# Kernel optimization log

Hardware: AMD Instinct MI355X
Metric: run time of the kernel (lower is better)

## Reference

```python
import jax, jax.numpy as jnp
import numpy as np

B, H, S, D = 2, 12, 2048, 64

def setup_inputs() -> dict:
    key = jax.random.key(0)
    kq, kk, kv = jax.random.split(key, 3)
    Q = jax.random.normal(kq, (B, H, S, D), dtype=jnp.float32)
    K = jax.random.normal(kk, (B, H, S, D), dtype=jnp.float32)
    V = jax.random.normal(kv, (B, H, S, D), dtype=jnp.float32)
    return {"Q": Q, "K": K, "V": V}

def reference(Q, K, V):
    # NOTE: original code scales by sqrt(Q.shape[-2]) (the sequence length),
    # not the head dim — reproduced faithfully.
    scale = 1.0 / np.sqrt(Q.shape[-2]).astype(np.float32)
    scores = jnp.einsum('bhqd,bhkd->bhqk', Q, K) * scale  # [B,H,S,S]
    attn = jax.nn.softmax(scores, axis=-1)
    context = jnp.einsum('bhqk,bhkd->bhqd', attn, V)      # [B,H,S,D]
    # torch .squeeze(-1) only removes the last dim if it is size 1; D=64 so no-op
    return context
```

## Files before the change

### kernel.cpp

```cpp
#include <hip/hip_runtime.h>
#include <hip/hip_bf16.h>
#include <math.h>
#include <stdint.h>

#define BATCH 2
#define NH 12
#define SEQ 2048
#define HD 64
#define TQ 64
#define TK 64
#define NHEADS (BATCH*NH)
#define NIT (SEQ / TK)

typedef short bf16x8 __attribute__((ext_vector_type(8)));
typedef float f32x4 __attribute__((ext_vector_type(4)));
typedef float f32x16 __attribute__((ext_vector_type(16)));
typedef unsigned short us4_t __attribute__((ext_vector_type(4)));
typedef unsigned short us8_t __attribute__((ext_vector_type(8)));
typedef unsigned int u32x4 __attribute__((ext_vector_type(4)));

#if __has_builtin(__builtin_amdgcn_exp2f)
#define EXP2F(x) __builtin_amdgcn_exp2f(x)
#else
#define EXP2F(x) exp2f(x)
#endif

static __device__ __forceinline__ unsigned short f2bf(float f) {
    unsigned int u = __float_as_uint(f);
    u += 0x7fffu + ((u >> 16) & 1u);
    return (unsigned short)(u >> 16);
}

static __device__ __forceinline__ unsigned int pack2bf(float a, float b) {
    __hip_bfloat162 v = __float22bfloat162_rn(float2{a, b});
    return *(unsigned int*)&v;
}

static __device__ __forceinline__ void async_cp16(const void* g, void* l) {
    __builtin_amdgcn_global_load_lds(
        (const __attribute__((address_space(1))) void*)g,
        (__attribute__((address_space(3))) void*)(uintptr_t)l,
        16, 0, 0);
}

static __device__ __forceinline__ int tile_off(int r, int c) {
    int rp  = r >> 1;
    int pos = (((r & 1) << 3) | c) ^ (rp & 15);
    return rp * 128 + pos * 8;
}

__global__ __launch_bounds__(256)
void prep_kv(const float* __restrict__ K, const float* __restrict__ V,
             unsigned short* __restrict__ Kb, unsigned short* __restrict__ Vtb) {
    __shared__ unsigned short T[64][66];
    const int bh = blockIdx.x >> 5;
    const int s0 = (blockIdx.x & 31) * 64;
    const int tid = threadIdx.x;
    const size_t off = ((size_t)bh * SEQ + s0) * HD;

    #pragma unroll
    for (int u = 0; u < 4; ++u) {
        int idx = u * 1024 + tid * 4;
        float4 a = *(const float4*)&K[off + idx];
        us4_t r4 = { f2bf(a.x), f2bf(a.y), f2bf(a.z), f2bf(a.w) };
        *(us4_t*)&Kb[off + idx] = r4;
    }
    #pragma unroll
    for (int u = 0; u < 4; ++u) {
        int idx = u * 1024 + tid * 4;
        int r = idx >> 6, col = idx & 63;
        float4 a = *(const float4*)&V[off + idx];
        *(unsigned int*)&T[r][col]     = pack2bf(a.x, a.y);
        *(unsigned int*)&T[r][col + 2] = pack2bf(a.z, a.w);
    }
    __syncthreads();
    unsigned short* Vdst = Vtb + (size_t)bh * HD * SEQ;
    const int g = tid & 7, dd = tid >> 3;
    #pragma unroll
    for (int h = 0; h < 2; ++h) {
        int d = dd + 32 * h;
        us8_t r8;
        #pragma unroll
        for (int j = 0; j < 8; ++j) {
            int src = ((g >> 1) << 4) + ((j >> 2) << 3) + ((g & 1) << 2) + (j & 3);
            r8[j] = T[src][d];
        }
        *(us8_t*)&Vdst[(size_t)d * SEQ + s0 + g * 8] = r8;
    }
}

__global__ __launch_bounds__(256, 3)
void fa_main(const float* __restrict__ Q,
             const unsigned short* __restrict__ Kb,
             const unsigned short* __restrict__ Vtb,
             float* __restrict__ O, float qs) {
    const int x  = blockIdx.x & 7;
    const int t  = blockIdx.x >> 3;
    const int bh = x + 8 * (t % 3);
    const int qt = t / 3;
    const int q0 = qt * TQ;

    __shared__ __align__(16) unsigned char SH[49664];
    float* Lsum = (float*)(SH + 49152);
    float* Linv = (float*)(SH + 49408);
    float* ORed = (float*)SH;
    unsigned short* QS = (unsigned short*)(SH + 32768);

    const int tid  = threadIdx.x;
    const int w    = tid >> 6;
    const int mt   = w >> 1;
    const int nt   = w & 1;
    const int lane = tid & 63;
    const int l31  = lane & 31;
    const int hi   = lane >> 5;

    const float*          Qh = Q   + ((size_t)bh * SEQ + q0) * HD;
    const unsigned short* Kh = Kb  + (size_t)bh * SEQ * HD;
    const unsigned short* Vh = Vtb + (size_t)bh * HD * SEQ;

    int rS[2], cS[2];
    #pragma unroll
    for (int i = 0; i < 2; ++i) {
        int rp = w * 8 + 4 * i + (lane >> 4);
        int lc = (lane & 15) ^ (rp & 15);
        rS[i] = 2 * rp + (lc >> 3);
        cS[i] = lc & 7;
    }
    const int dst0 = (w * 8 + 0) * 128, dst1 = (w * 8 + 4) * 128;
    const size_t kG0 = (size_t)rS[0] * HD  + cS[0] * 8;
    const size_t kG1 = (size_t)rS[1] * HD  + cS[1] * 8;
    const size_t vG0 = (size_t)rS[0] * SEQ + cS[0] * 8;
    const size_t vG1 = (size_t)rS[1] * SEQ + cS[1] * 8;

    {
        unsigned short* K0 = (unsigned short*)(SH);
        unsigned short* V0 = (unsigned short*)(SH + 8192);
        async_cp16(Kh + kG0, &K0[dst0]);
        async_cp16(Kh + kG1, &K0[dst1]);
        async_cp16(Vh + vG0, &V0[dst0]);
        async_cp16(Vh + vG1, &V0[dst1]);
    }
    #pragma unroll
    for (int u = 0; u < 4; ++u) {
        int idx = u * 1024 + tid * 4;
        int r = idx >> 6, col = idx & 63;
        float4 a = *(const float4*)&Qh[idx];
        uint2 pk = { pack2bf(a.x * qs, a.y * qs), pack2bf(a.z * qs, a.w * qs) };
        *(uint2*)&QS[tile_off(r, col >> 3) + (col & 7)] = pk;
    }
    __syncthreads();

    bf16x8 qf[4];
    #pragma unroll
    for (int s = 0; s < 4; ++s)
        qf[s] = *(const bf16x8*)&QS[tile_off(mt * 32 + l31, s * 2 + hi)];
    __syncthreads();

    {
        unsigned short* K1 = (unsigned short*)(SH + 16384);
        unsigned short* V1 = (unsigned short*)(SH + 16384 + 8192);
        async_cp16(Kh + (size_t)TK * HD + kG0, &K1[dst0]);
        async_cp16(Kh + (size_t)TK * HD + kG1, &K1[dst1]);
        async_cp16(Vh + (size_t)TK + vG0,      &V1[dst0]);
        async_cp16(Vh + (size_t)TK + vG1,      &V1[dst1]);
    }

    int kOffL[4], vOffL[2][2];
    #pragma unroll
    for (int s = 0; s < 4; ++s) kOffL[s] = tile_off(nt * 32 + l31, s * 2 + hi);
    #pragma unroll
    for (int dt = 0; dt < 2; ++dt)
        #pragma unroll
        for (int ks = 0; ks < 2; ++ks)
            vOffL[dt][ks] = tile_off(dt * 32 + l31, nt * 4 + ks * 2 + hi);

    f32x16 o[2];
    o[0] = (f32x16)(0.f);
    o[1] = (f32x16)(0.f);
    float lsum = 0.f;

    auto FIN = [&](const f32x16& sp, const bf16x8 (&vp)[2][2]) {
        float e0[8], e1[8];
        #pragma unroll
        for (int r = 0; r < 8; ++r) e0[r] = EXP2F(sp[r]);
        #pragma unroll
        for (int r = 0; r < 8; ++r) e1[r] = EXP2F(sp[8 + r]);
        union { u32x4 d; bf16x8 h; } pu0, pu1;
        pu0.d = (u32x4){ pack2bf(e0[0], e0[1]), pack2bf(e0[2], e0[3]),
                         pack2bf(e0[4], e0[5]), pack2bf(e0[6], e0[7]) };
        pu1.d = (u32x4){ pack2bf(e1[0], e1[1]), pack2bf(e1[2], e1[3]),
                         pack2bf(e1[4], e1[5]), pack2bf(e1[6], e1[7]) };
        bf16x8 pf0 = pu0.h, pf1 = pu1.h;
        o[0] = __builtin_amdgcn_mfma_f32_32x32x16_bf16(pf0, vp[0][0], o[0], 0, 0, 0);
        o[1] = __builtin_amdgcn_mfma_f32_32x32x16_bf16(pf0, vp[1][0], o[1], 0, 0, 0);
        o[0] = __builtin_amdgcn_mfma_f32_32x32x16_bf16(pf1, vp[0][1], o[0], 0, 0, 0);
        o[1] = __builtin_amdgcn_mfma_f32_32x32x16_bf16(pf1, vp[1][1], o[1], 0, 0, 0);
        float t0 = ((e0[0] + e0[1]) + (e0[2] + e0[3]))
                 + ((e0[4] + e0[5]) + (e0[6] + e0[7]));
        float t1 = ((e1[0] + e1[1]) + (e1[2] + e1[3]))
                 + ((e1[4] + e1[5]) + (e1[6] + e1[7]));
        lsum += t0 + t1;
    };

    unsigned int b0 = 0, b1 = 16384, b2 = 32768;

    f32x16 scp;
    bf16x8 vfp[2][2];

    {
        unsigned short* Kn = (unsigned short*)(SH + b2);
        unsigned short* Vn = (unsigned short*)(SH + b2 + 8192);
        async_cp16(Kh + (size_t)2 * TK * HD + kG0, &Kn[dst0]);
        async_cp16(Kh + (size_t)2 * TK * HD + kG1, &Kn[dst1]);
        async_cp16(Vh + (size_t)2 * TK + vG0,      &Vn[dst0]);
        async_cp16(Vh + (size_t)2 * TK + vG1,      &Vn[dst1]);

        const unsigned short* Ks = (const unsigned short*)(SH + b0);
        const unsigned short* Vs = (const unsigned short*)(SH + b0 + 8192);
        #pragma unroll
        for (int dt = 0; dt < 2; ++dt)
            #pragma unroll
            for (int ks = 0; ks < 2; ++ks)
                vfp[dt][ks] = *(const bf16x8*)&Vs[vOffL[dt][ks]];
        f32x16 sc = (f32x16)(0.f);
        #pragma unroll
        for (int s = 0; s < 4; ++s) {
            bf16x8 kf = *(const bf16x8*)&Ks[kOffL[s]];
            sc = __builtin_amdgcn_mfma_f32_32x32x16_bf16(kf, qf[s], sc, 0, 0, 0);
        }
        scp = sc;
        unsigned int btmp = b0; b0 = b1; b1 = b2; b2 = btmp;
    }

    #pragma unroll 2
    for (int it = 1; it < NIT; ++it) {
        asm volatile("s_waitcnt lgkmcnt(0)" ::: "memory");
        if (it == NIT - 1) { asm volatile("s_waitcnt vmcnt(0)" ::: "memory"); }
        else               { asm volatile("s_waitcnt vmcnt(4)" ::: "memory"); }
        __builtin_amdgcn_s_barrier();

        if (it + 2 < NIT) {
            const size_t kv = (size_t)(it + 2) * TK;
            unsigned short* Kn = (unsigned short*)(SH + b2);
            unsigned short* Vn = (unsigned short*)(SH + b2 + 8192);
            async_cp16(Kh + kv * HD + kG0, &Kn[dst0]);
            async_cp16(Kh + kv * HD + kG1, &Kn[dst1]);
            async_cp16(Vh + kv + vG0,      &Vn[dst0]);
            async_cp16(Vh + kv + vG1,      &Vn[dst1]);
        }
        const unsigned short* Ks = (const unsigned short*)(SH + b0);
        const unsigned short* Vs = (const unsigned short*)(SH + b0 + 8192);

        bf16x8 vfc[2][2];
        #pragma unroll
        for (int dt = 0; dt < 2; ++dt)
            #pragma unroll
            for (int ks = 0; ks < 2; ++ks)
                vfc[dt][ks] = *(const bf16x8*)&Vs[vOffL[dt][ks]];

        f32x16 scc = (f32x16)(0.f);
        #pragma unroll
        for (int s = 0; s < 4; ++s) {
            bf16x8 kf = *(const bf16x8*)&Ks[kOffL[s]];
            scc = __builtin_amdgcn_mfma_f32_32x32x16_bf16(kf, qf[s], scc, 0, 0, 0);
        }
        FIN(scp, vfp);

        scp = scc;
        #pragma unroll
        for (int dt = 0; dt < 2; ++dt)
            #pragma unroll
            for (int ks = 0; ks < 2; ++ks)
                vfp[dt][ks] = vfc[dt][ks];

        unsigned int btmp = b0; b0 = b1; b1 = b2; b2 = btmp;
    }

    FIN(scp, vfp);

    lsum += __shfl_xor(lsum, 32, 64);

    if (nt == 1) {
        if (lane < 32) Lsum[mt * 32 + lane] = lsum;
        #pragma unroll
        for (int dt = 0; dt < 2; ++dt) {
            const int d = dt * 32 + l31;
            #pragma unroll
            for (int g = 0; g < 4; ++g) {
                const int m0 = mt * 32 + 8 * g + 4 * hi;
                const int ph = (m0 >> 2) ^ (d & 15);
                float4 v = { o[dt][4*g+0], o[dt][4*g+1], o[dt][4*g+2], o[dt][4*g+3] };
                *(float4*)&ORed[d * 64 + ph * 4] = v;
            }
        }
    }
    __syncthreads();

    if (nt == 0) {
        float ltot = lsum + Lsum[mt * 32 + l31];
        if (lane < 32) Linv[mt * 32 + lane] = 1.0f / ltot;
        float* Oh = O + ((size_t)bh * SEQ + q0) * HD;
        #pragma unroll
        for (int dt = 0; dt < 2; ++dt) {
            const int d = dt * 32 + l31;
            #pragma unroll
            for (int g = 0; g < 4; ++g) {
                const int m0 = mt * 32 + 8 * g + 4 * hi;
                const int ph = (m0 >> 2) ^ (d & 15);
                float4 part = *(const float4*)&ORed[d * 64 + ph * 4];
                float4 inv4 = *(const float4*)&Linv[m0];
                const float* pp = (const float*)&part;
                const float* ii = (const float*)&inv4;
                #pragma unroll
                for (int j = 0; j < 4; ++j)
                    Oh[(size_t)(m0 + j) * HD + d] = (o[dt][4*g+j] + pp[j]) * ii[j];
            }
        }
    }
}

#define PAD 8
#define LSTR (HD + PAD)

__global__ __launch_bounds__(256)
void fa_fwd_fb(const float* __restrict__ Q, const float* __restrict__ K,
               const float* __restrict__ V, float* __restrict__ O) {
    const int x  = blockIdx.x & 7;
    const int t  = blockIdx.x >> 3;
    const int bh = x + 8 * (t % 3);
    const int qt = t / 3;
    const int q0 = qt * TQ;
    const long base = (long)bh * SEQ * HD;

    __shared__ unsigned short Qs[TQ][LSTR];
    __shared__ unsigned short Ks2[64][LSTR];
    __shared__ unsigned short Vt[HD][64 + PAD];
    __shared__ unsigned short Ps2[4][16][LSTR];

    const int tid  = threadIdx.x;
    const int wave = tid >> 6;
    const int lane = tid & 63;
    const int col  = lane & 15;
    const int quad = lane >> 4;
    const int m0   = wave * 16;

    #pragma unroll
    for (int i = 0; i < 4; ++i) {
        int idx = tid + 256 * i;
        int row = idx >> 4;
        int c4  = (idx & 15) * 4;
        float4 v = *(const float4*)&Q[base + (long)(q0 + row) * HD + c4];
        ushort4 b = { f2bf(v.x), f2bf(v.y), f2bf(v.z), f2bf(v.w) };
        *(ushort4*)&Qs[row][c4] = b;
    }
    __syncthreads();

    bf16x8 aq0 = *(const bf16x8*)&Qs[m0 + col][quad * 8];
    bf16x8 aq1 = *(const bf16x8*)&Qs[m0 + col][32 + quad * 8];

    f32x4 o0 = {0.f,0.f,0.f,0.f}, o1 = o0, o2 = o0, o3 = o0;
    float l[4] = {0.f, 0.f, 0.f, 0.f};
    const float scale = 0.022097086912079608f;

    for (int kv0 = 0; kv0 < SEQ; kv0 += 64) {
        __syncthreads();
        #pragma unroll
        for (int i = 0; i < 4; ++i) {
            int idx = tid + 256 * i;
            int row = idx >> 4;
            int c4  = (idx & 15) * 4;
            float4 kv = *(const float4*)&K[base + (long)(kv0 + row) * HD + c4];
            ushort4 kb = { f2bf(kv.x), f2bf(kv.y), f2bf(kv.z), f2bf(kv.w) };
            *(ushort4*)&Ks2[row][c4] = kb;
            float4 vv = *(const float4*)&V[base + (long)(kv0 + row) * HD + c4];
            Vt[c4 + 0][row] = f2bf(vv.x);
            Vt[c4 + 1][row] = f2bf(vv.y);
            Vt[c4 + 2][row] = f2bf(vv.z);
            Vt[c4 + 3][row] = f2bf(vv.w);
        }
        __syncthreads();

        f32x4 sc[4];
        #pragma unroll
        for (int n = 0; n < 4; ++n) {
            bf16x8 b0 = *(const bf16x8*)&Ks2[n * 16 + col][quad * 8];
            bf16x8 b1 = *(const bf16x8*)&Ks2[n * 16 + col][32 + quad * 8];
            f32x4 acc = {0.f,0.f,0.f,0.f};
            acc = __builtin_amdgcn_mfma_f32_16x16x32_bf16(aq0, b0, acc, 0, 0, 0);
            acc = __builtin_amdgcn_mfma_f32_16x16x32_bf16(aq1, b1, acc, 0, 0, 0);
            sc[n] = acc;
        }

        float tsum[4] = {0.f, 0.f, 0.f, 0.f};
        #pragma unroll
        for (int n = 0; n < 4; ++n) {
            #pragma unroll
            for (int r = 0; r < 4; ++r) {
                float p = __expf(sc[n][r] * scale);
                tsum[r] += p;
                Ps2[wave][quad * 4 + r][n * 16 + col] = f2bf(p);
            }
        }
        #pragma unroll
        for (int off = 1; off < 16; off <<= 1) {
            #pragma unroll
            for (int r = 0; r < 4; ++r) tsum[r] += __shfl_xor(tsum[r], off, 64);
        }
        #pragma unroll
        for (int r = 0; r < 4; ++r) l[r] += tsum[r];

        bf16x8 ap0 = *(const bf16x8*)&Ps2[wave][col][quad * 8];
        bf16x8 ap1 = *(const bf16x8*)&Ps2[wave][col][32 + quad * 8];
        #pragma unroll
        for (int n = 0; n < 4; ++n) {
            bf16x8 b0 = *(const bf16x8*)&Vt[n * 16 + col][quad * 8];
            bf16x8 b1 = *(const bf16x8*)&Vt[n * 16 + col][32 + quad * 8];
            f32x4* op = (n == 0) ? &o0 : (n == 1) ? &o1 : (n == 2) ? &o2 : &o3;
            *op = __builtin_amdgcn_mfma_f32_16x16x32_bf16(ap0, b0, *op, 0, 0, 0);
            *op = __builtin_amdgcn_mfma_f32_16x16x32_bf16(ap1, b1, *op, 0, 0, 0);
        }
    }

    float inv[4];
    #pragma unroll
    for (int r = 0; r < 4; ++r) inv[r] = 1.0f / l[r];
    #pragma unroll
    for (int r = 0; r < 4; ++r) {
        long row = base + (long)(q0 + m0 + quad * 4 + r) * HD;
        O[row +  0 + col] = o0[r] * inv[r];
        O[row + 16 + col] = o1[r] * inv[r];
        O[row + 32 + col] = o2[r] * inv[r];
        O[row + 48 + col] = o3[r] * inv[r];
    }
}

extern "C" void kernel_launch(void* const* d_in, const int* in_sizes, int n_in,
                              void* d_out, int out_size, void* d_ws, size_t ws_size,
                              hipStream_t stream) {
    const float* Q = (const float*)d_in[0];
    const float* K = (const float*)d_in[1];
    const float* V = (const float*)d_in[2];
    float* O = (float*)d_out;

    const size_t tensorElems = (size_t)NHEADS * SEQ * HD;
    const size_t need = 2 * tensorElems * sizeof(unsigned short);

    if (ws_size >= need) {
        unsigned short* Kb  = (unsigned short*)d_ws;
        unsigned short* Vtb = Kb + tensorElems;
        const float qs = (float)(1.4426950408889634 / sqrt(2048.0));
        prep_kv<<<dim3(NHEADS * (SEQ / 64)), dim3(256), 0, stream>>>(K, V, Kb, Vtb);
        fa_main<<<dim3(NHEADS * (SEQ / TQ)), dim3(256), 0, stream>>>(Q, Kb, Vtb, O, qs);
    } else {
        fa_fwd_fb<<<dim3(NHEADS * (SEQ / TQ)), dim3(256), 0, stream>>>(Q, K, V, O);
    }
}
```

Measured before the change: 115.8 us.

## Fuse K/V bf16 prep into attention kernel with grid-wide atomic barrier

```diff
diff --git a/kernel.cpp b/kernel.cpp
--- a/kernel.cpp
+++ b/kernel.cpp
@@ -11,6 +11,7 @@
 #define TK 64
 #define NHEADS (BATCH*NH)
 #define NIT (SEQ / TK)
+#define NBLK (NHEADS * (SEQ / TQ))
 
 typedef short bf16x8 __attribute__((ext_vector_type(8)));
 typedef float f32x4 __attribute__((ext_vector_type(4)));
@@ -49,64 +50,62 @@
     return rp * 128 + pos * 8;
 }
 
-__global__ __launch_bounds__(256)
-void prep_kv(const float* __restrict__ K, const float* __restrict__ V,
-             unsigned short* __restrict__ Kb, unsigned short* __restrict__ Vtb) {
-    __shared__ unsigned short T[64][66];
-    const int bh = blockIdx.x >> 5;
-    const int s0 = (blockIdx.x & 31) * 64;
+__global__ __launch_bounds__(256, 3)
+void fa_all(const float* __restrict__ Q, const float* __restrict__ K,
+            const float* __restrict__ V,
+            unsigned short* __restrict__ Kb, unsigned short* __restrict__ Vtb,
+            unsigned int* __restrict__ cnt, float* __restrict__ O, float qs) {
+    __shared__ __align__(16) unsigned char SH[49664];
     const int tid = threadIdx.x;
-    const size_t off = ((size_t)bh * SEQ + s0) * HD;
-
-    #pragma unroll
-    for (int u = 0; u < 4; ++u) {
-        int idx = u * 1024 + tid * 4;
-        float4 a = *(const float4*)&K[off + idx];
-        us4_t r4 = { f2bf(a.x), f2bf(a.y), f2bf(a.z), f2bf(a.w) };
-        *(us4_t*)&Kb[off + idx] = r4;
-    }
-    #pragma unroll
-    for (int u = 0; u < 4; ++u) {
-        int idx = u * 1024 + tid * 4;
-        int r = idx >> 6, col = idx & 63;
-        float4 a = *(const float4*)&V[off + idx];
-        *(unsigned int*)&T[r][col]     = pack2bf(a.x, a.y);
-        *(unsigned int*)&T[r][col + 2] = pack2bf(a.z, a.w);
-    }
-    __syncthreads();
-    unsigned short* Vdst = Vtb + (size_t)bh * HD * SEQ;
-    const int g = tid & 7, dd = tid >> 3;
-    #pragma unroll
-    for (int h = 0; h < 2; ++h) {
-        int d = dd + 32 * h;
-        us8_t r8;
-        #pragma unroll
-        for (int j = 0; j < 8; ++j) {
-            int src = ((g >> 1) << 4) + ((j >> 2) << 3) + ((g & 1) << 2) + (j & 3);
-            r8[j] = T[src][d];
-        }
-        *(us8_t*)&Vdst[(size_t)d * SEQ + s0 + g * 8] = r8;
-    }
-}
-
-__global__ __launch_bounds__(256, 3)
-void fa_main(const float* __restrict__ Q,
-             const unsigned short* __restrict__ Kb,
-             const unsigned short* __restrict__ Vtb,
-             float* __restrict__ O, float qs) {
+
+    {
+        unsigned short (*T)[66] = (unsigned short (*)[66])SH;
+        const int bhp = blockIdx.x >> 5;
+        const int s0p = (blockIdx.x & 31) * 64;
+        const size_t offp = ((size_t)bhp * SEQ + s0p) * HD;
+
+        #pragma unroll
+        for (int u = 0; u < 4; ++u) {
+            int idx = u * 1024 + tid * 4;
+            float4 a = *(const float4*)&K[offp + idx];
+            us4_t r4 = { f2bf(a.x), f2bf(a.y), f2bf(a.z), f2bf(a.w) };
+            *(us4_t*)&Kb[offp + idx] = r4;
+        }
+        #pragma unroll
+        for (int u = 0; u < 4; ++u) {
+            int idx = u * 1024 + tid * 4;
+            int r = idx >> 6, col = idx & 63;
+            float4 a = *(const float4*)&V[offp + idx];
+            *(unsigned int*)&T[r][col]     = pack2bf(a.x, a.y);
+            *(unsigned int*)&T[r][col + 2] = pack2bf(a.z, a.w);
+        }
+        __syncthreads();
+        unsigned short* Vdst = Vtb + (size_t)bhp * HD * SEQ;
+        const int g = tid & 7, dd = tid >> 3;
+        #pragma unroll
+        for (int h = 0; h < 2; ++h) {
+            int d = dd + 32 * h;
+            us8_t r8;
+            #pragma unroll
+            for (int j = 0; j < 8; ++j) {
+                int src = ((g >> 1) << 4) + ((j >> 2) << 3) + ((g & 1) << 2) + (j & 3);
+                r8[j] = T[src][d];
+            }
+            *(us8_t*)&Vdst[(size_t)d * SEQ + s0p + g * 8] = r8;
+        }
+    }
+
     const int x  = blockIdx.x & 7;
     const int t  = blockIdx.x >> 3;
     const int bh = x + 8 * (t % 3);
     const int qt = t / 3;
     const int q0 = qt * TQ;
 
-    __shared__ __align__(16) unsigned char SH[49664];
     float* Lsum = (float*)(SH + 49152);
     float* Linv = (float*)(SH + 49408);
     float* ORed = (float*)SH;
     unsigned short* QS = (unsigned short*)(SH + 32768);
 
-    const int tid  = threadIdx.x;
     const int w    = tid >> 6;
     const int mt   = w >> 1;
     const int nt   = w & 1;
@@ -131,6 +130,33 @@
     const size_t kG1 = (size_t)rS[1] * HD  + cS[1] * 8;
     const size_t vG0 = (size_t)rS[0] * SEQ + cS[0] * 8;
     const size_t vG1 = (size_t)rS[1] * SEQ + cS[1] * 8;
+
+    #pragma unroll
+    for (int u = 0; u < 4; ++u) {
+        int idx = u * 1024 + tid * 4;
+        int r = idx >> 6, col = idx & 63;
+        float4 a = *(const float4*)&Qh[idx];
+        uint2 pk = { pack2bf(a.x * qs, a.y * qs), pack2bf(a.z * qs, a.w * qs) };
+        *(uint2*)&QS[tile_off(r, col >> 3) + (col & 7)] = pk;
+    }
+    __syncthreads();
+
+    bf16x8 qf[4];
+    #pragma unroll
+    for (int s = 0; s < 4; ++s)
+        qf[s] = *(const bf16x8*)&QS[tile_off(mt * 32 + l31, s * 2 + hi)];
+    __syncthreads();
+
+    if (tid == 0) {
+        __builtin_amdgcn_fence(__ATOMIC_RELEASE, "agent");
+        __hip_atomic_fetch_add(cnt, 1u, __ATOMIC_RELEASE, __HIP_MEMORY_SCOPE_AGENT);
+        while (__hip_atomic_load(cnt, __ATOMIC_ACQUIRE, __HIP_MEMORY_SCOPE_AGENT)
+               < (unsigned int)NBLK) {
+            __builtin_amdgcn_s_sleep(8);
+        }
+        __builtin_amdgcn_fence(__ATOMIC_ACQUIRE, "agent");
+    }
+    __syncthreads();
 
     {
         unsigned short* K0 = (unsigned short*)(SH);
@@ -139,24 +165,6 @@
         async_cp16(Kh + kG1, &K0[dst1]);
         async_cp16(Vh + vG0, &V0[dst0]);
         async_cp16(Vh + vG1, &V0[dst1]);
-    }
-    #pragma unroll
-    for (int u = 0; u < 4; ++u) {
-        int idx = u * 1024 + tid * 4;
-        int r = idx >> 6, col = idx & 63;
-        float4 a = *(const float4*)&Qh[idx];
-        uint2 pk = { pack2bf(a.x * qs, a.y * qs), pack2bf(a.z * qs, a.w * qs) };
-        *(uint2*)&QS[tile_off(r, col >> 3) + (col & 7)] = pk;
-    }
-    __syncthreads();
-
-    bf16x8 qf[4];
-    #pragma unroll
-    for (int s = 0; s < 4; ++s)
-        qf[s] = *(const bf16x8*)&QS[tile_off(mt * 32 + l31, s * 2 + hi)];
-    __syncthreads();
-
-    {
         unsigned short* K1 = (unsigned short*)(SH + 16384);
         unsigned short* V1 = (unsigned short*)(SH + 16384 + 8192);
         async_cp16(Kh + (size_t)TK * HD + kG0, &K1[dst0]);
@@ -164,6 +172,8 @@
         async_cp16(Vh + (size_t)TK + vG0,      &V1[dst0]);
         async_cp16(Vh + (size_t)TK + vG1,      &V1[dst1]);
     }
+    asm volatile("s_waitcnt vmcnt(4)" ::: "memory");
+    __builtin_amdgcn_s_barrier();
 
     int kOffL[4], vOffL[2][2];
     #pragma unroll
@@ -443,14 +453,15 @@
     float* O = (float*)d_out;
 
     const size_t tensorElems = (size_t)NHEADS * SEQ * HD;
-    const size_t need = 2 * tensorElems * sizeof(unsigned short);
+    const size_t need = 2 * tensorElems * sizeof(unsigned short) + 64;
 
     if (ws_size >= need) {
         unsigned short* Kb  = (unsigned short*)d_ws;
         unsigned short* Vtb = Kb + tensorElems;
+        unsigned int* cnt   = (unsigned int*)(Vtb + tensorElems);
+        hipMemsetAsync(cnt, 0, sizeof(unsigned int), stream);
         const float qs = (float)(1.4426950408889634 / sqrt(2048.0));
-        prep_kv<<<dim3(NHEADS * (SEQ / 64)), dim3(256), 0, stream>>>(K, V, Kb, Vtb);
-        fa_main<<<dim3(NHEADS * (SEQ / TQ)), dim3(256), 0, stream>>>(Q, Kb, Vtb, O, qs);
+        fa_all<<<dim3(NBLK), dim3(256), 0, stream>>>(Q, K, V, Kb, Vtb, cnt, O, qs);
     } else {
         fa_fwd_fb<<<dim3(NHEADS * (SEQ / TQ)), dim3(256), 0, stream>>>(Q, K, V, O);
     }
```

Measured after the change: 216.5 us. 1.87x slower.
